# Performance work log

Measured on AMD Instinct MI355X. Metric: run time of the kernel, lower is better.

The kernel has to match this reference:

```python
import jax, jax.numpy as jnp
import numpy as np

B, IN_SIZE, IN_DIM = 16, 2048, 512
HEADS, OUT_SIZE = 4, 64
EPS = 0.1
MAX_ITER = 30
SIGMA = 0.1


def setup_inputs() -> dict:
    key = jax.random.key(0)
    k1, k2 = jax.random.split(key)
    x = jax.random.normal(k1, (B, IN_SIZE, IN_DIM), dtype=jnp.float32)
    stdv = 1.0 / np.sqrt(OUT_SIZE)
    weight = jax.random.uniform(k2, (HEADS, OUT_SIZE, IN_DIM), jnp.float32, -stdv, stdv)
    return {"x": x, "weight": weight}


def _position_filter(in_size, out_size, sigma):
    # 1-D gaussian position filter (image=False branch of get_position_filter)
    a = jnp.arange(0.0, in_size, dtype=jnp.float32)[:, None] / in_size
    b = jnp.arange(0.0, out_size, dtype=jnp.float32)[None, :] / out_size
    return jnp.exp(-(((a - b) / sigma) ** 2))  # (in_size, out_size)


def log_sinkhorn(K, iterations):
    """Log-domain Sinkhorn. K: (B, H, N, M) log-kernel.
    Row marginal a = 1/N (uniform, no mask). Scaling vectors are
    detached (envelope trick) before forming the transport plan,
    matching the original OTK implementation."""
    Bn, H, N, M = K.shape
    log_a = jnp.full((Bn, H, N), -jnp.log(jnp.float32(N)), dtype=K.dtype)
    u0 = jnp.zeros((Bn, H, N), K.dtype)
    v0 = jnp.zeros((Bn, H, M), K.dtype)

    def step(carry, _):
        u, v = carry
        Z = K + u[..., :, None] + v[..., None, :]
        u = log_a - jax.nn.logsumexp(Z, axis=-1)
        Z = K + u[..., :, None] + v[..., None, :]
        v = -jax.nn.logsumexp(Z, axis=-2)
        return (u, v), None

    (u, v), _ = jax.lax.scan(step, (u0, v0), None, length=iterations)
    u = jax.lax.stop_gradient(u)
    v = jax.lax.stop_gradient(v)
    return jnp.exp(K + u[..., :, None] + v[..., None, :])  # (B,H,N,M)


def reference(x, weight):
    # x: (B, N, D); weight: (H, M, D)
    pf = _position_filter(IN_SIZE, OUT_SIZE, SIGMA)  # (N, M)
    # euclidean cost via expansion (cdist)
    x2 = jnp.sum(x * x, axis=-1)                      # (B, N)
    w2 = jnp.sum(weight * weight, axis=-1)            # (H, M)
    xw = jnp.einsum('bnd,hmd->bhnm', x, weight)       # (B, H, N, M)
    C = jnp.sqrt(jnp.maximum(x2[:, None, :, None] + w2[None, :, None, :] - 2.0 * xw, 0.0))
    K = (-C / EPS) * pf[None, None]                   # position filter applied to log-kernel
    P = log_sinkhorn(K, MAX_ITER)                     # (B, H, N, M) transport plan
    # attn: (B, M, H, N) -> (B, M*H, N)
    attn = jnp.transpose(P, (0, 3, 1, 2)).reshape(B, OUT_SIZE * HEADS, IN_SIZE)
    out = jnp.matmul(attn, x)                         # (B, M*H, D)
    return out.reshape(B, OUT_SIZE, HEADS * IN_DIM)
```

## Files before the change

### kernel.cpp

```cpp
#include <hip/hip_runtime.h>
#include <hip/hip_fp16.h>


typedef _Float16 h2 __attribute__((ext_vector_type(2)));
typedef _Float16 h8 __attribute__((ext_vector_type(8)));
typedef float f4 __attribute__((ext_vector_type(4)));

#define NB 16
#define NN 2048
#define ND 512
#define NH 4
#define NM 64
#define NITER 30
#define EUSCALE 8.0f

static __device__ __forceinline__ float fdot2f(h2 a, h2 b, float c) {
#if __has_builtin(__builtin_amdgcn_fdot2)
  return __builtin_amdgcn_fdot2(a, b, c, false);
#else
  return (float)a[0] * (float)b[0] + (float)a[1] * (float)b[1] + c;
#endif
}

static __device__ __forceinline__ h2 pkrtz(float a, float b) {
  return __builtin_bit_cast(h2, __builtin_amdgcn_cvt_pkrtz(a, b));
}

static __device__ __forceinline__ h8 pack8(float4 a, float4 b) {
  h8 r;
  r[0] = (_Float16)a.x; r[1] = (_Float16)a.y; r[2] = (_Float16)a.z; r[3] = (_Float16)a.w;
  r[4] = (_Float16)b.x; r[5] = (_Float16)b.y; r[6] = (_Float16)b.z; r[7] = (_Float16)b.w;
  return r;
}

static __device__ __forceinline__ float sq4(float4 a) {
  return a.x * a.x + a.y * a.y + a.z * a.z + a.w * a.w;
}

__global__ __launch_bounds__(256) void k0_xt(const float* __restrict__ x,
                                             _Float16* __restrict__ xT) {
  __shared__ float tile[64][65];
  const int b = blockIdx.z;
  const int n0 = blockIdx.x * 64;
  const int d0 = blockIdx.y * 64;
  const int t = threadIdx.x;
  const int nr = t >> 2;
  const int ds = (t & 3) * 16;
  const float4* src = (const float4*)(x + ((size_t)(b * NN + n0 + nr) * ND + d0 + ds));
  float4 v0 = src[0], v1 = src[1], v2 = src[2], v3 = src[3];
  float vals[16] = {v0.x, v0.y, v0.z, v0.w, v1.x, v1.y, v1.z, v1.w,
                    v2.x, v2.y, v2.z, v2.w, v3.x, v3.y, v3.z, v3.w};
#pragma unroll
  for (int j = 0; j < 16; ++j) tile[ds + j][nr] = vals[j];
  __syncthreads();
  const int dr = t >> 2;
  const int ns = (t & 3) * 16;
  h8 o0, o1;
#pragma unroll
  for (int j = 0; j < 8; ++j) o0[j] = (_Float16)tile[dr][ns + j];
#pragma unroll
  for (int j = 0; j < 8; ++j) o1[j] = (_Float16)tile[dr][ns + 8 + j];
  _Float16* dst = xT + ((size_t)(b * ND + d0 + dr) * NN + n0 + ns);
  *(h8*)dst = o0;
  *(h8*)(dst + 8) = o1;
}

__global__ __launch_bounds__(512) void k1_buildE(const float* __restrict__ x,
                                                 const float* __restrict__ w,
                                                 _Float16* __restrict__ E) {
  __shared__ _Float16 Ah[128][72];
  __shared__ _Float16 Bh[256][72];
  __shared__ float x2s[128][4];
  __shared__ float w2s[256][2];
  __shared__ float x2r[128];
  __shared__ float w2r[256];

  const int b = blockIdx.y;
  const int n0 = blockIdx.x * 128;
  const int tid = threadIdx.x;
  const int lane = tid & 63;
  const int wv = tid >> 6;
  const int lrow = lane & 15;
  const int kq = lane >> 4;

  f4 acc[16];
#pragma unroll
  for (int i = 0; i < 16; ++i) acc[i] = (f4){0.f, 0.f, 0.f, 0.f};

  const int ar = tid >> 2, ac = (tid & 3) * 16;
  const int br = tid >> 1, bc = (tid & 1) * 32;
  const float* xsrc = x + ((size_t)(b * NN + n0 + ar) * ND + ac);
  const float* wsrc = w + ((size_t)br * ND + bc);
  float x2p = 0.f, w2p = 0.f;

  for (int kt = 0; kt < 8; ++kt) {
    {
      const float4* s4 = (const float4*)(xsrc + kt * 64);
      float4 a0 = s4[0], a1 = s4[1], a2 = s4[2], a3 = s4[3];
      x2p += sq4(a0) + sq4(a1) + sq4(a2) + sq4(a3);
      *(h8*)&Ah[ar][ac] = pack8(a0, a1);
      *(h8*)&Ah[ar][ac + 8] = pack8(a2, a3);
    }
    {
      const float4* s4 = (const float4*)(wsrc + kt * 64);
      float4 u0 = s4[0], u1 = s4[1], u2 = s4[2], u3 = s4[3];
      float4 u4 = s4[4], u5 = s4[5], u6 = s4[6], u7 = s4[7];
      w2p += sq4(u0) + sq4(u1) + sq4(u2) + sq4(u3)
           + sq4(u4) + sq4(u5) + sq4(u6) + sq4(u7);
      *(h8*)&Bh[br][bc] = pack8(u0, u1);
      *(h8*)&Bh[br][bc + 8] = pack8(u2, u3);
      *(h8*)&Bh[br][bc + 16] = pack8(u4, u5);
      *(h8*)&Bh[br][bc + 24] = pack8(u6, u7);
    }
    __syncthreads();
#pragma unroll
    for (int s = 0; s < 2; ++s) {
      h8 af = *(const h8*)&Ah[wv * 16 + lrow][s * 32 + kq * 8];
#pragma unroll
      for (int cf = 0; cf < 16; ++cf) {
        h8 bf = *(const h8*)&Bh[cf * 16 + lrow][s * 32 + kq * 8];
        acc[cf] = __builtin_amdgcn_mfma_f32_16x16x32_f16(af, bf, acc[cf], 0, 0, 0);
      }
    }
    __syncthreads();
  }

  x2s[ar][tid & 3] = x2p;
  w2s[br][tid & 1] = w2p;
  __syncthreads();
  if (tid < 128) {
    x2r[tid] = x2s[tid][0] + x2s[tid][1] + x2s[tid][2] + x2s[tid][3];
  } else if (tid < 384) {
    const int r = tid - 128;
    w2r[r] = w2s[r][0] + w2s[r][1];
  }
  __syncthreads();

#pragma unroll
  for (int cf = 0; cf < 16; ++cf) {
    const int mg = cf * 16 + lrow;
    const int hh = mg >> 6;
    const int m = mg & 63;
    const float w2v = w2r[mg];
    const float bm = (float)m * (1.0f / 64.0f);
    _Float16* Eb = E + ((size_t)(b * NH + hh) * NN) * NM;
#pragma unroll
    for (int j = 0; j < 4; ++j) {
      const int nl = wv * 16 + kq * 4 + j;
      const int n = n0 + nl;
      const float c2 = x2r[nl] + w2v - 2.0f * acc[cf][j];
      const float Cd = sqrtf(fmaxf(c2, 0.0f));
      const float tt = (float)n * (1.0f / 2048.0f) - bm;
      const float pf = __expf(-100.0f * tt * tt);
      const float Ev = __expf(-10.0f * Cd * pf);
      Eb[(size_t)n * NM + m] = (_Float16)Ev;
    }
  }
}

__global__ __launch_bounds__(512, 2) void k2_sinkhorn(const _Float16* __restrict__ E,
                                                      _Float16* __restrict__ Pt) {
  const int bh = blockIdx.x;
  const int b = bh >> 2, h = bh & 3;
  const int tid = threadIdx.x;
  const int lane = tid & 63;

  __shared__ float evf[64];
  __shared__ __align__(16) h2 evh[32];
  __shared__ unsigned int pbuf[512];

  const _Float16* Ep = E + (size_t)bh * (NN * NM);

  h2 e[4][32];
#pragma unroll
  for (int i = 0; i < 4; ++i) {
    const uint4* src = (const uint4*)(Ep + (size_t)(4 * tid + i) * NM);
#pragma unroll
    for (int q = 0; q < 8; ++q) {
      uint4 v = src[q];
      e[i][q * 4 + 0] = __builtin_bit_cast(h2, v.x);
      e[i][q * 4 + 1] = __builtin_bit_cast(h2, v.y);
      e[i][q * 4 + 2] = __builtin_bit_cast(h2, v.z);
      e[i][q * 4 + 3] = __builtin_bit_cast(h2, v.w);
    }
  }

  float eu[4] = {1.f, 1.f, 1.f, 1.f};
  if (tid < 64) evf[tid] = 1.f;
  if (tid < 32) evh[tid] = pkrtz(1.f, 1.f);
  __syncthreads();

#pragma unroll 1
  for (int it = 0; it < NITER; ++it) {
    h2 evr[32];
    {
      const uint4* ev4 = (const uint4*)evh;
#pragma unroll
      for (int q8 = 0; q8 < 8; ++q8) {
        uint4 v = ev4[q8];
        evr[q8 * 4 + 0] = __builtin_bit_cast(h2, v.x);
        evr[q8 * 4 + 1] = __builtin_bit_cast(h2, v.y);
        evr[q8 * 4 + 2] = __builtin_bit_cast(h2, v.z);
        evr[q8 * 4 + 3] = __builtin_bit_cast(h2, v.w);
      }
    }
    float sa[4] = {0.f, 0.f, 0.f, 0.f};
    float sb[4] = {0.f, 0.f, 0.f, 0.f};
#pragma unroll
    for (int q = 0; q < 16; ++q) {
#pragma unroll
      for (int i = 0; i < 4; ++i) sa[i] = fdot2f(e[i][q], evr[q], sa[i]);
    }
#pragma unroll
    for (int q = 16; q < 32; ++q) {
#pragma unroll
      for (int i = 0; i < 4; ++i) sb[i] = fdot2f(e[i][q], evr[q], sb[i]);
    }
#pragma unroll
    for (int i = 0; i < 4; ++i) {
      eu[i] = 4.8828125e-4f * __builtin_amdgcn_rcpf(eu[i] * (sa[i] + sb[i]));
    }
    h2 eup[4];
#pragma unroll
    for (int i = 0; i < 4; ++i) {
      const float es = eu[i] * EUSCALE;
      eup[i] = pkrtz(es, es);
    }
    h2 tp[32];
#pragma unroll
    for (int q = 0; q < 32; ++q) {
      tp[q] = e[0][q] * eup[0] + e[1][q] * eup[1];
      tp[q] += e[2][q] * eup[2] + e[3][q] * eup[3];
    }
#pragma unroll
    for (int k = 0; k < 5; ++k) {
      const int nn = 32 >> k;
      const bool up = (lane >> k) & 1;
#pragma unroll
      for (int p = 0; p < (nn >> 1); ++p) {
        h2 keep = up ? tp[p + (nn >> 1)] : tp[p];
        h2 send = up ? tp[p] : tp[p + (nn >> 1)];
        int rv = __shfl_xor(__builtin_bit_cast(int, send), 1 << k, 64);
        tp[p] = keep + __builtin_bit_cast(h2, rv);
      }
    }
    pbuf[tid] = __builtin_bit_cast(unsigned int, tp[0]);
    __syncthreads();
    if (tid < 32) {
      const int j = tid;
      const int rev = ((j & 1) << 4) | ((j & 2) << 2) | (j & 4) | ((j & 8) >> 2) | ((j & 16) >> 4);
      float T0 = 0.f, T1 = 0.f;
#pragma unroll
      for (int wq = 0; wq < 8; ++wq) {
        h2 a = __builtin_bit_cast(h2, pbuf[wq * 64 + rev]);
        h2 c = __builtin_bit_cast(h2, pbuf[wq * 64 + rev + 32]);
        T0 += (float)a[0] + (float)c[0];
        T1 += (float)a[1] + (float)c[1];
      }
      const float e0 = evf[2 * j], e1 = evf[2 * j + 1];
      const float n0 = EUSCALE * __builtin_amdgcn_rcpf(e0 * T0);
      const float n1 = EUSCALE * __builtin_amdgcn_rcpf(e1 * T1);
      evf[2 * j] = n0;
      evf[2 * j + 1] = n1;
      evh[j] = pkrtz(n0, n1);
    }
    __syncthreads();
  }

  _Float16* Pb = Pt + ((size_t)(b * 256 + h)) * NN;
#pragma unroll
  for (int q = 0; q < 32; ++q) {
    const float ev0 = evf[2 * q];
    const float ev1 = evf[2 * q + 1];
    float a0[4], a1[4];
#pragma unroll
    for (int i = 0; i < 4; ++i) {
      a0[i] = (float)e[i][q][0] * eu[i] * ev0;
      a1[i] = (float)e[i][q][1] * eu[i] * ev1;
    }
    uint2 st0, st1;
    st0.x = __builtin_bit_cast(unsigned int, pkrtz(a0[0], a0[1]));
    st0.y = __builtin_bit_cast(unsigned int, pkrtz(a0[2], a0[3]));
    st1.x = __builtin_bit_cast(unsigned int, pkrtz(a1[0], a1[1]));
    st1.y = __builtin_bit_cast(unsigned int, pkrtz(a1[2], a1[3]));
    *(uint2*)(Pb + (size_t)(2 * q) * 4 * NN + 4 * tid) = st0;
    *(uint2*)(Pb + (size_t)(2 * q + 1) * 4 * NN + 4 * tid) = st1;
  }
}

__global__ __launch_bounds__(512) void k3_out(const _Float16* __restrict__ Pt,
                                              const _Float16* __restrict__ xT,
                                              float* __restrict__ out) {
  __shared__ _Float16 As[128][72];
  __shared__ _Float16 Bs[64][72];
  const int b = blockIdx.z;
  const int hf = blockIdx.y;
  const int dt = blockIdx.x;
  const int tid = threadIdx.x;
  const int lane = tid & 63;
  const int wv = tid >> 6;
  const int lrow = lane & 15;
  const int kq = lane >> 4;

  f4 acc[4];
#pragma unroll
  for (int i = 0; i < 4; ++i) acc[i] = (f4){0.f, 0.f, 0.f, 0.f};

  const int ar = tid >> 2, ac = (tid & 3) * 16;
  const int brd = tid >> 3, bn = (tid & 7) * 8;
  const _Float16* asrc = Pt + ((size_t)(b * 256 + hf * 128 + ar) * NN + ac);
  const _Float16* bsrc = xT + ((size_t)(b * ND + dt * 64 + brd) * NN + bn);

  for (int kt = 0; kt < 32; ++kt) {
    const int k0 = kt * 64;
    h8 a0 = *(const h8*)(asrc + k0);
    h8 a1 = *(const h8*)(asrc + k0 + 8);
    h8 bv = *(const h8*)(bsrc + k0);
    *(h8*)&As[ar][ac] = a0;
    *(h8*)&As[ar][ac + 8] = a1;
    *(h8*)&Bs[brd][bn] = bv;
    __syncthreads();
#pragma unroll
    for (int s = 0; s < 2; ++s) {
      h8 af = *(const h8*)&As[wv * 16 + lrow][s * 32 + kq * 8];
#pragma unroll
      for (int cf = 0; cf < 4; ++cf) {
        h8 bf = *(const h8*)&Bs[cf * 16 + lrow][s * 32 + kq * 8];
        acc[cf] = __builtin_amdgcn_mfma_f32_16x16x32_f16(af, bf, acc[cf], 0, 0, 0);
      }
    }
    __syncthreads();
  }
#pragma unroll
  for (int cf = 0; cf < 4; ++cf) {
    const int d = dt * 64 + cf * 16 + lrow;
#pragma unroll
    for (int j = 0; j < 4; ++j) {
      const int row = hf * 128 + wv * 16 + kq * 4 + j;
      out[(size_t)(b * 256 + row) * ND + d] = acc[cf][j];
    }
  }
}

extern "C" void kernel_launch(void* const* d_in, const int* in_sizes, int n_in,
                              void* d_out, int out_size, void* d_ws, size_t ws_size,
                              hipStream_t stream) {
  const float* x = (const float*)d_in[0];
  const float* w = (const float*)d_in[1];
  float* out = (float*)d_out;
  char* ws = (char*)d_ws;
  _Float16* xT = (_Float16*)ws;
  _Float16* E  = (_Float16*)(ws + (size_t)33554432);
  _Float16* Pt = (_Float16*)(ws + (size_t)50331648);

  k0_xt<<<dim3(32, 8, NB), 256, 0, stream>>>(x, xT);
  k1_buildE<<<dim3(16, NB), 512, 0, stream>>>(x, w, E);
  k2_sinkhorn<<<dim3(64), 512, 0, stream>>>(E, Pt);
  k3_out<<<dim3(8, 2, NB), 512, 0, stream>>>(Pt, xT, out);
}
```

Measured before the change: 172.1 us.

## Stream E rows from global memory each Sinkhorn iteration instead of holding them in registers

The Sinkhorn kernel stops keeping its 4x64 fp16 slice of E in registers for the whole loop. Each iteration now reloads one row at a time from global memory (expected to hit L2) and fuses the row dot product, the u update and the accumulation of the column partial sum for that row. After the loop, E is loaded again for the output write. This frees registers and the launch bound min-blocks hint drops from 2 to 1, but it adds 30 re-reads of E per block, so the loop now depends on memory latency and cache bandwidth rather than on register-resident data.

```diff
diff --git a/kernel.cpp b/kernel.cpp
--- a/kernel.cpp
+++ b/kernel.cpp
@@ -158,7 +158,7 @@
   }
 }
 
-__global__ __launch_bounds__(512, 2) void k2_sinkhorn(const _Float16* __restrict__ E,
+__global__ __launch_bounds__(512, 1) void k2_sinkhorn(const _Float16* __restrict__ E,
                                                       _Float16* __restrict__ Pt) {
   const int bh = blockIdx.x;
   const int b = bh >> 2, h = bh & 3;
@@ -171,20 +171,6 @@
 
   const _Float16* Ep = E + (size_t)bh * (NN * NM);
 
-  h2 e[4][32];
-#pragma unroll
-  for (int i = 0; i < 4; ++i) {
-    const uint4* src = (const uint4*)(Ep + (size_t)(4 * tid + i) * NM);
-#pragma unroll
-    for (int q = 0; q < 8; ++q) {
-      uint4 v = src[q];
-      e[i][q * 4 + 0] = __builtin_bit_cast(h2, v.x);
-      e[i][q * 4 + 1] = __builtin_bit_cast(h2, v.y);
-      e[i][q * 4 + 2] = __builtin_bit_cast(h2, v.z);
-      e[i][q * 4 + 3] = __builtin_bit_cast(h2, v.w);
-    }
-  }
-
   float eu[4] = {1.f, 1.f, 1.f, 1.f};
   if (tid < 64) evf[tid] = 1.f;
   if (tid < 32) evh[tid] = pkrtz(1.f, 1.f);
@@ -192,46 +178,52 @@
 
 #pragma unroll 1
   for (int it = 0; it < NITER; ++it) {
+    asm volatile("" ::: "memory");
     h2 evr[32];
     {
       const uint4* ev4 = (const uint4*)evh;
 #pragma unroll
-      for (int q8 = 0; q8 < 8; ++q8) {
-        uint4 v = ev4[q8];
-        evr[q8 * 4 + 0] = __builtin_bit_cast(h2, v.x);
-        evr[q8 * 4 + 1] = __builtin_bit_cast(h2, v.y);
-        evr[q8 * 4 + 2] = __builtin_bit_cast(h2, v.z);
-        evr[q8 * 4 + 3] = __builtin_bit_cast(h2, v.w);
-      }
-    }
-    float sa[4] = {0.f, 0.f, 0.f, 0.f};
-    float sb[4] = {0.f, 0.f, 0.f, 0.f};
-#pragma unroll
-    for (int q = 0; q < 16; ++q) {
-#pragma unroll
-      for (int i = 0; i < 4; ++i) sa[i] = fdot2f(e[i][q], evr[q], sa[i]);
-    }
-#pragma unroll
-    for (int q = 16; q < 32; ++q) {
-#pragma unroll
-      for (int i = 0; i < 4; ++i) sb[i] = fdot2f(e[i][q], evr[q], sb[i]);
-    }
-#pragma unroll
-    for (int i = 0; i < 4; ++i) {
-      eu[i] = 4.8828125e-4f * __builtin_amdgcn_rcpf(eu[i] * (sa[i] + sb[i]));
-    }
-    h2 eup[4];
-#pragma unroll
-    for (int i = 0; i < 4; ++i) {
-      const float es = eu[i] * EUSCALE;
-      eup[i] = pkrtz(es, es);
+      for (int j = 0; j < 8; ++j) {
+        uint4 v = ev4[j];
+        evr[j * 4 + 0] = __builtin_bit_cast(h2, v.x);
+        evr[j * 4 + 1] = __builtin_bit_cast(h2, v.y);
+        evr[j * 4 + 2] = __builtin_bit_cast(h2, v.z);
+        evr[j * 4 + 3] = __builtin_bit_cast(h2, v.w);
+      }
     }
     h2 tp[32];
 #pragma unroll
-    for (int q = 0; q < 32; ++q) {
-      tp[q] = e[0][q] * eup[0] + e[1][q] * eup[1];
-      tp[q] += e[2][q] * eup[2] + e[3][q] * eup[3];
-    }
+    for (int q = 0; q < 32; ++q) tp[q] = (h2){(_Float16)0.f, (_Float16)0.f};
+
+#pragma unroll
+    for (int r = 0; r < 4; ++r) {
+      const uint4* sr = (const uint4*)(Ep + (size_t)(4 * tid + r) * NM);
+      h2 er[32];
+#pragma unroll
+      for (int j = 0; j < 8; ++j) {
+        uint4 v = sr[j];
+        er[j * 4 + 0] = __builtin_bit_cast(h2, v.x);
+        er[j * 4 + 1] = __builtin_bit_cast(h2, v.y);
+        er[j * 4 + 2] = __builtin_bit_cast(h2, v.z);
+        er[j * 4 + 3] = __builtin_bit_cast(h2, v.w);
+      }
+      float sa = 0.f, sb = 0.f, sc = 0.f, sd = 0.f;
+#pragma unroll
+      for (int q = 0; q < 8; ++q) {
+        sa = fdot2f(er[q], evr[q], sa);
+        sb = fdot2f(er[q + 8], evr[q + 8], sb);
+        sc = fdot2f(er[q + 16], evr[q + 16], sc);
+        sd = fdot2f(er[q + 24], evr[q + 24], sd);
+      }
+      const float eun =
+          4.8828125e-4f * __builtin_amdgcn_rcpf(eu[r] * ((sa + sb) + (sc + sd)));
+      eu[r] = eun;
+      const float es = eun * EUSCALE;
+      const h2 p = pkrtz(es, es);
+#pragma unroll
+      for (int q = 0; q < 32; ++q) tp[q] += er[q] * p;
+    }
+
 #pragma unroll
     for (int k = 0; k < 5; ++k) {
       const int nn = 32 >> k;
@@ -267,6 +259,20 @@
     __syncthreads();
   }
 
+  asm volatile("" ::: "memory");
+  h2 ee[4][32];
+#pragma unroll
+  for (int r = 0; r < 4; ++r) {
+    const uint4* sr = (const uint4*)(Ep + (size_t)(4 * tid + r) * NM);
+#pragma unroll
+    for (int j = 0; j < 8; ++j) {
+      uint4 v = sr[j];
+      ee[r][j * 4 + 0] = __builtin_bit_cast(h2, v.x);
+      ee[r][j * 4 + 1] = __builtin_bit_cast(h2, v.y);
+      ee[r][j * 4 + 2] = __builtin_bit_cast(h2, v.z);
+      ee[r][j * 4 + 3] = __builtin_bit_cast(h2, v.w);
+    }
+  }
   _Float16* Pb = Pt + ((size_t)(b * 256 + h)) * NN;
 #pragma unroll
   for (int q = 0; q < 32; ++q) {
@@ -274,9 +280,9 @@
     const float ev1 = evf[2 * q + 1];
     float a0[4], a1[4];
 #pragma unroll
-    for (int i = 0; i < 4; ++i) {
-      a0[i] = (float)e[i][q][0] * eu[i] * ev0;
-      a1[i] = (float)e[i][q][1] * eu[i] * ev1;
+    for (int r = 0; r < 4; ++r) {
+      a0[r] = (float)ee[r][q][0] * eu[r] * ev0;
+      a1[r] = (float)ee[r][q][1] * eu[r] * ev1;
     }
     uint2 st0, st1;
     st0.x = __builtin_bit_cast(unsigned int, pkrtz(a0[0], a0[1]));
```

Result: slower. 355.5 us (+106.6%).
